# Kernel optimization log

Measured on AMD Instinct MI355X. Metric: run time of the kernel, lower is better.

## Reference

```python
import jax, jax.numpy as jnp
import numpy as np

N = 100000      # nodes
E = 3200000     # edges (avg degree 32)
DIN, DH, DOUT = 128, 32, 2


def setup_inputs() -> dict:
    key = jax.random.key(0)
    k1, k2, k3, k4 = jax.random.split(key, 4)
    x = jax.random.normal(k1, (N, DIN), dtype=jnp.float32)
    edge_index = jax.random.randint(k2, (2, E), 0, N, dtype=jnp.int64)
    # Glorot-ish scaled weights
    W1 = jax.random.normal(k3, (DIN, DH), dtype=jnp.float32) / np.sqrt(DIN)
    b1 = jnp.zeros((DH,), dtype=jnp.float32)
    W2 = jax.random.normal(k4, (DH, DOUT), dtype=jnp.float32) / np.sqrt(DH)
    b2 = jnp.zeros((DOUT,), dtype=jnp.float32)
    return {"x": x, "edge_index": edge_index, "W1": W1, "b1": b1, "W2": W2, "b2": b2}


def reference(x, edge_index, W1, b1, W2, b2):
    n = x.shape[0]
    # GCNConv default: add self-loops, symmetric deg^{-1/2} A deg^{-1/2} normalization
    loops = jnp.arange(n, dtype=edge_index.dtype)
    src = jnp.concatenate([edge_index[0], loops])  # [E+N]
    dst = jnp.concatenate([edge_index[1], loops])  # [E+N]
    deg = jax.ops.segment_sum(jnp.ones_like(dst, dtype=x.dtype), dst, num_segments=n)
    dinv = jnp.where(deg > 0, jax.lax.rsqrt(deg), 0.0)
    norm = dinv[src] * dinv[dst]  # [E+N]

    def gcn_layer(h, W, b):
        m = h @ W                                   # [n, dout] transform first (PyG order)
        msgs = m[src] * norm[:, None]               # gather + scale  [E+N, dout]
        agg = jax.ops.segment_sum(msgs, dst, num_segments=n)  # scatter-add
        return agg + b

    h = jax.nn.relu(gcn_layer(x, W1, b1))
    return gcn_layer(h, W2, b2)
```

## Files before the change

kernel.cpp:

```cpp
#include <hip/hip_runtime.h>
#include <hip/hip_bf16.h>

#define DIN 128
#define DH 32
#define DOUT 2
#define NPB 128
#define NPB_SHIFT 7
#define NBUK_MAX 1024
#define FILL_EDGES 8192
#define CHUNKB 8192


__device__ inline unsigned short f2bf(float f) {
    unsigned int u = __float_as_uint(f);
    u = (u + 0x7FFFu + ((u >> 16) & 1u)) >> 16;
    return (unsigned short)u;
}
__device__ inline float bf2f(unsigned short b) {
    return __uint_as_float(((unsigned int)b) << 16);
}
__device__ inline float bfLO(unsigned int w) { return __uint_as_float(w << 16); }
__device__ inline float bfHI(unsigned int w) { return __uint_as_float(w & 0xFFFF0000u); }

__global__ void zero_gcnt_kernel(int* __restrict__ gcnt, int nbuk) {
    int i = blockIdx.x * blockDim.x + threadIdx.x;
    if (i < nbuk) gcnt[i] = 0;
}

__global__ void bukhist_kernel(const int* __restrict__ dst, int* __restrict__ gcnt,
                               int e, int nbuk) {
    __shared__ int lcnt[NBUK_MAX];
    int t = threadIdx.x;
    for (int i = t; i < nbuk; i += 256) lcnt[i] = 0;
    __syncthreads();
    int e0 = blockIdx.x * FILL_EDGES;
    int m = min(FILL_EDGES, e - e0);
    for (int i = t; i < m; i += 256) atomicAdd(&lcnt[dst[e0 + i] >> NPB_SHIFT], 1);
    __syncthreads();
    for (int i = t; i < nbuk; i += 256)
        if (lcnt[i]) atomicAdd(&gcnt[i], lcnt[i]);
}

__global__ void scan_kernel(const int* __restrict__ gcnt, int* __restrict__ gbase,
                            int* __restrict__ gcur, int nbuk,
                            unsigned short* __restrict__ mqc, int n) {
    __shared__ int sd[256];
    int t = threadIdx.x;
    if (t < 16) ((unsigned int*)(mqc + (size_t)n * DH))[t] = 0u;
    int v[4], s = 0;
#pragma unroll
    for (int k = 0; k < 4; ++k) {
        int i = 4 * t + k;
        v[k] = (i < nbuk) ? gcnt[i] : 0;
        s += v[k];
    }
    sd[t] = s;
    __syncthreads();
    for (int off = 1; off < 256; off <<= 1) {
        int x = (t >= off) ? sd[t - off] : 0;
        __syncthreads();
        sd[t] += x;
        __syncthreads();
    }
    int run = sd[t] - s;
#pragma unroll
    for (int k = 0; k < 4; ++k) {
        int i = 4 * t + k;
        if (i < nbuk) { gbase[i] = run; gcur[i] = run; }
        run += v[k];
    }
}

__global__ void binfill_kernel(const int* __restrict__ src, const int* __restrict__ dst,
                               int* __restrict__ gcur, unsigned int* __restrict__ binned,
                               int e, int nbuk) {
    __shared__ int cnt[NBUK_MAX];
    __shared__ int pos[NBUK_MAX];
    __shared__ int gb[NBUK_MAX];
    __shared__ unsigned int sorted[FILL_EDGES];
    __shared__ unsigned short aux[FILL_EDGES];
    __shared__ int stmp[256];

    int t = threadIdx.x;
    int e0 = blockIdx.x * FILL_EDGES;
    int m = min(FILL_EDGES, e - e0);

    for (int i = t; i < nbuk; i += 256) cnt[i] = 0;
    __syncthreads();
    for (int i = t; i < m; i += 256) atomicAdd(&cnt[dst[e0 + i] >> NPB_SHIFT], 1);
    __syncthreads();

    int v[4], s = 0;
#pragma unroll
    for (int k = 0; k < 4; ++k) {
        int i = 4 * t + k;
        v[k] = (i < nbuk) ? cnt[i] : 0;
        s += v[k];
    }
    stmp[t] = s;
    __syncthreads();
    for (int off = 1; off < 256; off <<= 1) {
        int x = (t >= off) ? stmp[t - off] : 0;
        __syncthreads();
        stmp[t] += x;
        __syncthreads();
    }
    int run = stmp[t] - s;
#pragma unroll
    for (int k = 0; k < 4; ++k) {
        int i = 4 * t + k;
        if (i < nbuk) pos[i] = run;
        run += v[k];
    }
    __syncthreads();

    for (int i = t; i < m; i += 256) {
        int d = dst[e0 + i];
        int sv = src[e0 + i];
        int b = d >> NPB_SHIFT;
        int r = atomicAdd(&pos[b], 1);
        sorted[r] = ((unsigned int)(d & (NPB - 1)) << 17) | (unsigned int)sv;
        aux[r] = (unsigned short)b;
    }
    __syncthreads();

    for (int b = t; b < nbuk; b += 256) {
        int c = cnt[b];
        gb[b] = c ? atomicAdd(&gcur[b], c) : 0;
    }
    __syncthreads();

    for (int i = t; i < m; i += 256) {
        int b = aux[i];
        int start = pos[b] - cnt[b];
        binned[gb[b] + (i - start)] = sorted[i];
    }
}

__global__ void bdinv_kernel(const int* __restrict__ gbase, const int* __restrict__ gcnt,
                             const unsigned int* __restrict__ binned,
                             float* __restrict__ dinv, int* __restrict__ degarr, int n) {
    __shared__ int cnt[NPB];
    int t = threadIdx.x;
    int b = blockIdx.x;
    if (t < NPB) cnt[t] = 0;
    __syncthreads();
    const int beg = gbase[b];
    const int cntb = gcnt[b];
    for (int i = t; i < cntb; i += 256) atomicAdd(&cnt[binned[beg + i] >> 17], 1);
    __syncthreads();
    if (t < NPB) {
        int r = (b << NPB_SHIFT) + t;
        if (r < n) { dinv[r] = rsqrtf((float)(cnt[t] + 1)); degarr[r] = cnt[t]; }
    }
}

#define XLD 132
__global__ void gemm1_kernel(const float* __restrict__ x, const float* __restrict__ W1,
                             const float* __restrict__ dinv,
                             unsigned short* __restrict__ mqc, int n) {
    __shared__ float  Xl[32 * XLD];
    __shared__ float4 Wl4[DIN * 8];

    int t = threadIdx.x;
    for (int i = t; i < DIN * 8; i += 256) Wl4[i] = ((const float4*)W1)[i];

    int rb = blockIdx.x * 32;
    for (int i = t; i < 32 * 32; i += 256) {
        int rr = i >> 5, c4 = i & 31;
        int gr = rb + rr;
        float4 v = make_float4(0.f, 0.f, 0.f, 0.f);
        if (gr < n) v = ((const float4*)x)[(size_t)gr * 32 + c4];
        ((float4*)Xl)[rr * 33 + c4] = v;
    }
    __syncthreads();

    const int lane = t & 7;
    const int row  = t >> 3;
    const float* xrow = &Xl[row * XLD];
    float4 acc = make_float4(0.f, 0.f, 0.f, 0.f);
#pragma unroll
    for (int k = 0; k < DIN; ++k) {
        float xv = xrow[k];
        float4 w = Wl4[k * 8 + lane];
        acc.x += xv * w.x; acc.y += xv * w.y;
        acc.z += xv * w.z; acc.w += xv * w.w;
    }
    int r = rb + row;
    if (r < n) {
        float di = dinv[r];
        ushort4 sv;
        sv.x = f2bf(acc.x * di); sv.y = f2bf(acc.y * di);
        sv.z = f2bf(acc.z * di); sv.w = f2bf(acc.w * di);
        *(ushort4*)&mqc[(size_t)r * DH + 4 * lane] = sv;
    }
}

__global__ void __launch_bounds__(256, 3)
agg1_kernel(const int* __restrict__ gbase, const int* __restrict__ gcnt,
            const int* __restrict__ degarr,
            unsigned int* __restrict__ binned,
            const unsigned short* __restrict__ mqc,
            const float* __restrict__ dinv,
            const float* __restrict__ b1, const float* __restrict__ W2,
            float2* __restrict__ m2q, int n) {
    __shared__ unsigned int sortedc[CHUNKB];
    __shared__ int dg[NPB];
    __shared__ int coffs[NPB];
    __shared__ int poffs[NPB];
    __shared__ int cur[NPB];
    __shared__ int gmax[16];
    __shared__ int pbase[16];
    __shared__ int stmp[256];
    __shared__ int padtot;

    const int t = threadIdx.x;
    const int b = blockIdx.x;
    const int beg = gbase[b];
    const int cntb = gcnt[b];
    const int r0 = b << NPB_SHIFT;

    if (t < NPB) {
        int r = r0 + t;
        dg[t] = (r < n) ? degarr[r] : 0;
    }
    __syncthreads();

    if (t < 16) {
        int mx = 0;
#pragma unroll
        for (int k = 0; k < 8; ++k) mx = max(mx, dg[t * 8 + k]);
        gmax[t] = mx;
    }
    int v = (t < NPB) ? dg[t] : 0;
    stmp[t] = v;
    __syncthreads();

    if (t == 0) {
        int run = 0;
#pragma unroll
        for (int g = 0; g < 16; ++g) { pbase[g] = run; run += 8 * gmax[g]; }
        padtot = run;
    }
    for (int o = 1; o < NPB; o <<= 1) {
        int xx = (t >= o) ? stmp[t - o] : 0;
        __syncthreads();
        stmp[t] += xx;
        __syncthreads();
    }
    if (t < NPB) coffs[t] = stmp[t] - v;
    __syncthreads();

    if (padtot <= CHUNKB && cntb <= CHUNKB) {
        if (t < NPB) {
            int p = pbase[t >> 3] + (t & 7) * gmax[t >> 3];
            poffs[t] = p;
            cur[t] = p;
        }
        __syncthreads();

        for (int i = t; i < padtot; i += 256) sortedc[i] = (unsigned int)n;
        __syncthreads();
        for (int i = t; i < cntb; i += 256) {
            unsigned int en = binned[beg + i];
            int p = atomicAdd(&cur[en >> 17], 1);
            sortedc[p] = en & 0x1FFFFu;
        }
        __syncthreads();

        const int g = t >> 4, l = t & 15;
        const int mk = gmax[g];
        int bq[8];
#pragma unroll
        for (int q = 0; q < 8; ++q) bq[q] = poffs[g * 8 + q];

        float aLo[8], aHi[8];
#pragma unroll
        for (int q = 0; q < 8; ++q) { aLo[q] = 0.f; aHi[q] = 0.f; }

        for (int u = 0; u < mk; ++u) {
            unsigned int sv[8];
#pragma unroll
            for (int q = 0; q < 8; ++q) sv[q] = sortedc[bq[q] + u];
            unsigned int w[8];
#pragma unroll
            for (int q = 0; q < 8; ++q)
                w[q] = ((const unsigned int*)(mqc + (size_t)sv[q] * DH))[l];
#pragma unroll
            for (int q = 0; q < 8; ++q) {
                aLo[q] += bfLO(w[q]);
                aHi[q] += bfHI(w[q]);
            }
        }

        {
            int j = t >> 1, hf = t & 1;
            int d = dg[j], cb = coffs[j], pb = poffs[j];
            for (int k = hf; k < d; k += 2)
                binned[beg + cb + k] = sortedc[pb + k];
        }

        float2 bb = ((const float2*)b1)[l];
        float4 w4 = ((const float4*)W2)[l];
#pragma unroll
        for (int q = 0; q < 8; ++q) {
            int r = r0 + g * 8 + q;
            if (r < n) {
                float di = dinv[r];
                unsigned int sw = ((const unsigned int*)(mqc + (size_t)r * DH))[l];
                float h0 = fmaxf(di * (aLo[q] + bfLO(sw)) + bb.x, 0.0f);
                float h1 = fmaxf(di * (aHi[q] + bfHI(sw)) + bb.y, 0.0f);
                float p0 = h0 * w4.x + h1 * w4.z;
                float p1 = h0 * w4.y + h1 * w4.w;
#pragma unroll
                for (int o = 8; o > 0; o >>= 1) {
                    p0 += __shfl_down(p0, o, 16);
                    p1 += __shfl_down(p1, o, 16);
                }
                if (l == 0) m2q[r] = make_float2(di * p0, di * p1);
            }
        }
        return;
    }

    {
        const int lane = t & 31;
        const int half = t >> 5;
        float acc[16];
#pragma unroll
        for (int q = 0; q < 16; ++q) acc[q] = 0.0f;

        for (int off = 0; off < cntb; off += CHUNKB) {
            const int m = min(CHUNKB, cntb - off);

            if (t < NPB) cur[t] = 0;
            __syncthreads();
            for (int i = t; i < m; i += 256)
                atomicAdd(&cur[binned[beg + off + i] >> 17], 1);
            __syncthreads();

            int vv = (t < NPB) ? cur[t] : 0;
            stmp[t] = vv;
            __syncthreads();
            for (int o = 1; o < NPB; o <<= 1) {
                int xx = (t >= o) ? stmp[t - o] : 0;
                __syncthreads();
                stmp[t] += xx;
                __syncthreads();
            }
            if (t < NPB) { dg[t] = vv; poffs[t] = stmp[t] - vv; cur[t] = stmp[t] - vv; }
            __syncthreads();

            for (int i = t; i < m; i += 256) {
                unsigned int en = binned[beg + off + i];
                int p = atomicAdd(&cur[en >> 17], 1);
                sortedc[p] = en & 0x1FFFFu;
            }
            __syncthreads();

            int e0q[16], kq[16];
            int maxk = 0;
#pragma unroll
            for (int q = 0; q < 16; ++q) {
                int j = q * 8 + half;
                e0q[q] = poffs[j];
                kq[q] = dg[j];
                maxk = max(maxk, kq[q]);
            }
            for (int u = 0; u < maxk; ++u) {
                float val[16];
#pragma unroll
                for (int q = 0; q < 16; ++q) {
                    int idx = min(e0q[q] + u, m - 1);
                    int s = (int)sortedc[idx];
                    val[q] = bf2f(mqc[(size_t)s * DH + lane]);
                }
#pragma unroll
                for (int q = 0; q < 16; ++q)
                    acc[q] += (u < kq[q]) ? val[q] : 0.0f;
            }
            __syncthreads();
        }

#pragma unroll
        for (int q = 0; q < 16; ++q) {
            const int j = q * 8 + half;
            const int r = r0 + j;
            if (r < n) {
                float di = dinv[r];
                float a = acc[q] + bf2f(mqc[(size_t)r * DH + lane]);
                float h = fmaxf(di * a + b1[lane], 0.0f);
                float p0 = h * W2[lane * DOUT + 0];
                float p1 = h * W2[lane * DOUT + 1];
#pragma unroll
                for (int o = 16; o > 0; o >>= 1) {
                    p0 += __shfl_down(p0, o, 32);
                    p1 += __shfl_down(p1, o, 32);
                }
                if (lane == 0) m2q[r] = make_float2(di * p0, di * p1);
            }
        }
        if (cntb <= CHUNKB) {
            for (int i = t; i < cntb; i += 256) binned[beg + i] = sortedc[i];
        }
    }
}

__global__ void agg2_kernel(const int* __restrict__ gbase, const int* __restrict__ gcnt,
                            const int* __restrict__ degarr,
                            const unsigned int* __restrict__ binned,
                            const float2* __restrict__ m2q,
                            const float* __restrict__ dinv, const float* __restrict__ b2,
                            float* __restrict__ out, int n) {
    __shared__ int dg[NPB];
    __shared__ int offs[NPB];
    __shared__ int stmp[256];
    __shared__ float a0s[NPB], a1s[NPB];

    const int t = threadIdx.x;
    const int b = blockIdx.x;
    const int beg = gbase[b];
    const int cntb = gcnt[b];
    const int r0 = b << NPB_SHIFT;

    if (cntb <= CHUNKB) {
        if (t < NPB) {
            int r = r0 + t;
            dg[t] = (r < n) ? degarr[r] : 0;
        }
        __syncthreads();
        int v = (t < NPB) ? dg[t] : 0;
        stmp[t] = v;
        __syncthreads();
        for (int o = 1; o < NPB; o <<= 1) {
            int xx = (t >= o) ? stmp[t - o] : 0;
            __syncthreads();
            stmp[t] += xx;
            __syncthreads();
        }
        if (t < NPB) offs[t] = stmp[t] - v;
        __syncthreads();

        int j = t >> 1, hf = t & 1;
        int d = dg[j], o = offs[j];
        int lo = o + (hf ? (d >> 1) : 0);
        int hi = o + (hf ? d : (d >> 1));
        float a0 = 0.f, a1 = 0.f;
        for (int i = lo; i < hi; ++i) {
            int s = (int)(binned[beg + i] & 0x1FFFFu);
            float2 vv = m2q[s];
            a0 += vv.x; a1 += vv.y;
        }
        a0 += __shfl_down(a0, 1, 2);
        a1 += __shfl_down(a1, 1, 2);
        if (hf == 0) {
            int r = r0 + j;
            if (r < n) {
                float di = dinv[r];
                float2 self = m2q[r];
                out[(size_t)r * DOUT + 0] = di * (a0 + self.x) + b2[0];
                out[(size_t)r * DOUT + 1] = di * (a1 + self.y) + b2[1];
            }
        }
    } else {
        for (int i = t; i < NPB; i += 256) { a0s[i] = 0.f; a1s[i] = 0.f; }
        __syncthreads();
        for (int i = t; i < cntb; i += 256) {
            unsigned int entry = binned[beg + i];
            int sv = (int)(entry & 0x1FFFFu);
            int dl = (int)(entry >> 17);
            float2 vv = m2q[sv];
            atomicAdd(&a0s[dl], vv.x);
            atomicAdd(&a1s[dl], vv.y);
        }
        __syncthreads();
        for (int rl = t; rl < NPB; rl += 256) {
            int r = r0 + rl;
            if (r < n) {
                float di = dinv[r];
                float2 self = m2q[r];
                out[(size_t)r * DOUT + 0] = di * (a0s[rl] + self.x) + b2[0];
                out[(size_t)r * DOUT + 1] = di * (a1s[rl] + self.y) + b2[1];
            }
        }
    }
}

extern "C" void kernel_launch(void* const* d_in, const int* in_sizes, int n_in,
                              void* d_out, int out_size, void* d_ws, size_t ws_size,
                              hipStream_t stream) {
    const float* x  = (const float*)d_in[0];
    const int*   ei = (const int*)d_in[1];
    const float* W1 = (const float*)d_in[2];
    const float* b1 = (const float*)d_in[3];
    const float* W2 = (const float*)d_in[4];
    const float* b2 = (const float*)d_in[5];
    float* out = (float*)d_out;

    const int n = in_sizes[0] / DIN;
    const int e = in_sizes[1] / 2;
    const int* src = ei;
    const int* dst = ei + e;
    const int nbuk = (n + NPB - 1) >> NPB_SHIFT;

    char* ws = (char*)d_ws;
    float* dinv   = (float*)ws;          ws += (size_t)n * 4;
    int* degarr   = (int*)ws;            ws += (size_t)n * 4;
    int* gcnt     = (int*)ws;            ws += NBUK_MAX * 4;
    int* gbase    = (int*)ws;            ws += NBUK_MAX * 4;
    int* gcur     = (int*)ws;            ws += NBUK_MAX * 4;
    unsigned int* binned = (unsigned int*)ws;   ws += (size_t)e * 4;
    unsigned short* mqc  = (unsigned short*)ws; ws += ((size_t)n + 1) * DH * 2;
    float2* m2q   = (float2*)ws;

    const int B = 256;
    const int fill_blocks = (e + FILL_EDGES - 1) / FILL_EDGES;

    zero_gcnt_kernel<<<(nbuk + B - 1) / B, B, 0, stream>>>(gcnt, nbuk);
    bukhist_kernel<<<fill_blocks, B, 0, stream>>>(dst, gcnt, e, nbuk);
    scan_kernel<<<1, B, 0, stream>>>(gcnt, gbase, gcur, nbuk, mqc, n);
    binfill_kernel<<<fill_blocks, B, 0, stream>>>(src, dst, gcur, binned, e, nbuk);
    bdinv_kernel<<<nbuk, B, 0, stream>>>(gbase, gcnt, binned, dinv, degarr, n);
    gemm1_kernel<<<(n + 31) / 32, B, 0, stream>>>(x, W1, dinv, mqc, n);
    agg1_kernel<<<nbuk, B, 0, stream>>>(gbase, gcnt, degarr, binned, mqc, dinv, b1, W2, m2q, n);
    agg2_kernel<<<nbuk, B, 0, stream>>>(gbase, gcnt, degarr, binned, m2q, dinv, b2, out, n);
}
```

Before: 250.2 us.

## Replace per-bucket LDS sort with shared-memory atomic accumulation in aggregation

Both aggregation kernels drop the in-block counting sort of each bucket's edges (degree arrays, prefix scans, padded per-row slots, binned write-back). Instead they stream the bucket's binned edges directly, gather the source features, and accumulate them with LDS float atomics into a padded per-row accumulator. Edge loads become nontemporal and are unrolled by four, degarr is removed, and occupancy hints rise to 4. This cuts the sort and scan overhead and the write-back traffic, but adds LDS atomic contention and makes the summation order non-deterministic.

After: 882.9 us. 253% more time.

```diff
diff --git a/kernel.cpp b/kernel.cpp
--- a/kernel.cpp
+++ b/kernel.cpp
@@ -8,16 +8,12 @@
 #define NPB_SHIFT 7
 #define NBUK_MAX 1024
 #define FILL_EDGES 8192
-#define CHUNKB 8192
 
 
 __device__ inline unsigned short f2bf(float f) {
     unsigned int u = __float_as_uint(f);
     u = (u + 0x7FFFu + ((u >> 16) & 1u)) >> 16;
     return (unsigned short)u;
-}
-__device__ inline float bf2f(unsigned short b) {
-    return __uint_as_float(((unsigned int)b) << 16);
 }
 __device__ inline float bfLO(unsigned int w) { return __uint_as_float(w << 16); }
 __device__ inline float bfHI(unsigned int w) { return __uint_as_float(w & 0xFFFF0000u); }
@@ -139,7 +135,7 @@
 
 __global__ void bdinv_kernel(const int* __restrict__ gbase, const int* __restrict__ gcnt,
                              const unsigned int* __restrict__ binned,
-                             float* __restrict__ dinv, int* __restrict__ degarr, int n) {
+                             float* __restrict__ dinv, int n) {
     __shared__ int cnt[NPB];
     int t = threadIdx.x;
     int b = blockIdx.x;
@@ -151,7 +147,7 @@
     __syncthreads();
     if (t < NPB) {
         int r = (b << NPB_SHIFT) + t;
-        if (r < n) { dinv[r] = rsqrtf((float)(cnt[t] + 1)); degarr[r] = cnt[t]; }
+        if (r < n) dinv[r] = rsqrtf((float)(cnt[t] + 1));
     }
 }
 
@@ -196,23 +192,14 @@
     }
 }
 
-__global__ void __launch_bounds__(256, 3)
+__global__ void __launch_bounds__(256, 4)
 agg1_kernel(const int* __restrict__ gbase, const int* __restrict__ gcnt,
-            const int* __restrict__ degarr,
-            unsigned int* __restrict__ binned,
+            const unsigned int* __restrict__ binned,
             const unsigned short* __restrict__ mqc,
             const float* __restrict__ dinv,
             const float* __restrict__ b1, const float* __restrict__ W2,
             float2* __restrict__ m2q, int n) {
-    __shared__ unsigned int sortedc[CHUNKB];
-    __shared__ int dg[NPB];
-    __shared__ int coffs[NPB];
-    __shared__ int poffs[NPB];
-    __shared__ int cur[NPB];
-    __shared__ int gmax[16];
-    __shared__ int pbase[16];
-    __shared__ int stmp[256];
-    __shared__ int padtot;
+    __shared__ float acc[NPB * 33];
 
     const int t = threadIdx.x;
     const int b = blockIdx.x;
@@ -220,268 +207,108 @@
     const int cntb = gcnt[b];
     const int r0 = b << NPB_SHIFT;
 
-    if (t < NPB) {
-        int r = r0 + t;
-        dg[t] = (r < n) ? degarr[r] : 0;
-    }
-    __syncthreads();
-
-    if (t < 16) {
-        int mx = 0;
-#pragma unroll
-        for (int k = 0; k < 8; ++k) mx = max(mx, dg[t * 8 + k]);
-        gmax[t] = mx;
-    }
-    int v = (t < NPB) ? dg[t] : 0;
-    stmp[t] = v;
-    __syncthreads();
-
-    if (t == 0) {
-        int run = 0;
-#pragma unroll
-        for (int g = 0; g < 16; ++g) { pbase[g] = run; run += 8 * gmax[g]; }
-        padtot = run;
-    }
-    for (int o = 1; o < NPB; o <<= 1) {
-        int xx = (t >= o) ? stmp[t - o] : 0;
-        __syncthreads();
-        stmp[t] += xx;
-        __syncthreads();
-    }
-    if (t < NPB) coffs[t] = stmp[t] - v;
-    __syncthreads();
-
-    if (padtot <= CHUNKB && cntb <= CHUNKB) {
-        if (t < NPB) {
-            int p = pbase[t >> 3] + (t & 7) * gmax[t >> 3];
-            poffs[t] = p;
-            cur[t] = p;
+    for (int i = t; i < NPB * 33; i += 256) acc[i] = 0.f;
+    __syncthreads();
+
+    const int g = t >> 4, l = t & 15;
+    const unsigned int* __restrict__ bp = binned + beg;
+    const unsigned int* __restrict__ mq32 = (const unsigned int*)mqc;
+
+    int i = g;
+    for (; i + 48 < cntb; i += 64) {
+        unsigned int e0 = __builtin_nontemporal_load(&bp[i]);
+        unsigned int e1 = __builtin_nontemporal_load(&bp[i + 16]);
+        unsigned int e2 = __builtin_nontemporal_load(&bp[i + 32]);
+        unsigned int e3 = __builtin_nontemporal_load(&bp[i + 48]);
+        unsigned int w0 = mq32[(e0 & 0x1FFFFu) * 16u + l];
+        unsigned int w1 = mq32[(e1 & 0x1FFFFu) * 16u + l];
+        unsigned int w2 = mq32[(e2 & 0x1FFFFu) * 16u + l];
+        unsigned int w3 = mq32[(e3 & 0x1FFFFu) * 16u + l];
+        int d0 = (int)(e0 >> 17) * 33 + 2 * l;
+        int d1 = (int)(e1 >> 17) * 33 + 2 * l;
+        int d2 = (int)(e2 >> 17) * 33 + 2 * l;
+        int d3 = (int)(e3 >> 17) * 33 + 2 * l;
+        atomicAdd(&acc[d0], bfLO(w0)); atomicAdd(&acc[d0 + 1], bfHI(w0));
+        atomicAdd(&acc[d1], bfLO(w1)); atomicAdd(&acc[d1 + 1], bfHI(w1));
+        atomicAdd(&acc[d2], bfLO(w2)); atomicAdd(&acc[d2 + 1], bfHI(w2));
+        atomicAdd(&acc[d3], bfLO(w3)); atomicAdd(&acc[d3 + 1], bfHI(w3));
+    }
+    for (; i < cntb; i += 16) {
+        unsigned int e0 = __builtin_nontemporal_load(&bp[i]);
+        unsigned int w0 = mq32[(e0 & 0x1FFFFu) * 16u + l];
+        int d0 = (int)(e0 >> 17) * 33 + 2 * l;
+        atomicAdd(&acc[d0], bfLO(w0)); atomicAdd(&acc[d0 + 1], bfHI(w0));
+    }
+    __syncthreads();
+
+    const int j = t >> 1, hf = t & 1;
+    const int r = r0 + j;
+    if (r < n) {
+        const float di = dinv[r];
+        const unsigned int* srow = mq32 + (size_t)r * 16 + hf * 8;
+        const float* ar = &acc[j * 33 + hf * 16];
+        float p0 = 0.f, p1 = 0.f;
+#pragma unroll
+        for (int k = 0; k < 8; ++k) {
+            unsigned int sw = srow[k];
+            int c = hf * 16 + 2 * k;
+            float h0 = fmaxf(di * (ar[2 * k]     + bfLO(sw)) + b1[c],     0.0f);
+            float h1 = fmaxf(di * (ar[2 * k + 1] + bfHI(sw)) + b1[c + 1], 0.0f);
+            p0 += h0 * W2[2 * c]     + h1 * W2[2 * c + 2];
+            p1 += h0 * W2[2 * c + 1] + h1 * W2[2 * c + 3];
         }
-        __syncthreads();
-
-        for (int i = t; i < padtot; i += 256) sortedc[i] = (unsigned int)n;
-        __syncthreads();
-        for (int i = t; i < cntb; i += 256) {
-            unsigned int en = binned[beg + i];
-            int p = atomicAdd(&cur[en >> 17], 1);
-            sortedc[p] = en & 0x1FFFFu;
-        }
-        __syncthreads();
-
-        const int g = t >> 4, l = t & 15;
-        const int mk = gmax[g];
-        int bq[8];
-#pragma unroll
-        for (int q = 0; q < 8; ++q) bq[q] = poffs[g * 8 + q];
-
-        float aLo[8], aHi[8];
-#pragma unroll
-        for (int q = 0; q < 8; ++q) { aLo[q] = 0.f; aHi[q] = 0.f; }
-
-        for (int u = 0; u < mk; ++u) {
-            unsigned int sv[8];
-#pragma unroll
-            for (int q = 0; q < 8; ++q) sv[q] = sortedc[bq[q] + u];
-            unsigned int w[8];
-#pragma unroll
-            for (int q = 0; q < 8; ++q)
-                w[q] = ((const unsigned int*)(mqc + (size_t)sv[q] * DH))[l];
-#pragma unroll
-            for (int q = 0; q < 8; ++q) {
-                aLo[q] += bfLO(w[q]);
-                aHi[q] += bfHI(w[q]);
-            }
-        }
-
-        {
-            int j = t >> 1, hf = t & 1;
-            int d = dg[j], cb = coffs[j], pb = poffs[j];
-            for (int k = hf; k < d; k += 2)
-                binned[beg + cb + k] = sortedc[pb + k];
-        }
-
-        float2 bb = ((const float2*)b1)[l];
-        float4 w4 = ((const float4*)W2)[l];
-#pragma unroll
-        for (int q = 0; q < 8; ++q) {
-            int r = r0 + g * 8 + q;
-            if (r < n) {
-                float di = dinv[r];
-                unsigned int sw = ((const unsigned int*)(mqc + (size_t)r * DH))[l];
-                float h0 = fmaxf(di * (aLo[q] + bfLO(sw)) + bb.x, 0.0f);
-                float h1 = fmaxf(di * (aHi[q] + bfHI(sw)) + bb.y, 0.0f);
-                float p0 = h0 * w4.x + h1 * w4.z;
-                float p1 = h0 * w4.y + h1 * w4.w;
-#pragma unroll
-                for (int o = 8; o > 0; o >>= 1) {
-                    p0 += __shfl_down(p0, o, 16);
-                    p1 += __shfl_down(p1, o, 16);
-                }
-                if (l == 0) m2q[r] = make_float2(di * p0, di * p1);
-            }
-        }
-        return;
-    }
-
-    {
-        const int lane = t & 31;
-        const int half = t >> 5;
-        float acc[16];
-#pragma unroll
-        for (int q = 0; q < 16; ++q) acc[q] = 0.0f;
-
-        for (int off = 0; off < cntb; off += CHUNKB) {
-            const int m = min(CHUNKB, cntb - off);
-
-            if (t < NPB) cur[t] = 0;
-            __syncthreads();
-            for (int i = t; i < m; i += 256)
-                atomicAdd(&cur[binned[beg + off + i] >> 17], 1);
-            __syncthreads();
-
-            int vv = (t < NPB) ? cur[t] : 0;
-            stmp[t] = vv;
-            __syncthreads();
-            for (int o = 1; o < NPB; o <<= 1) {
-                int xx = (t >= o) ? stmp[t - o] : 0;
-                __syncthreads();
-                stmp[t] += xx;
-                __syncthreads();
-            }
-            if (t < NPB) { dg[t] = vv; poffs[t] = stmp[t] - vv; cur[t] = stmp[t] - vv; }
-            __syncthreads();
-
-            for (int i = t; i < m; i += 256) {
-                unsigned int en = binned[beg + off + i];
-                int p = atomicAdd(&cur[en >> 17], 1);
-                sortedc[p] = en & 0x1FFFFu;
-            }
-            __syncthreads();
-
-            int e0q[16], kq[16];
-            int maxk = 0;
-#pragma unroll
-            for (int q = 0; q < 16; ++q) {
-                int j = q * 8 + half;
-                e0q[q] = poffs[j];
-                kq[q] = dg[j];
-                maxk = max(maxk, kq[q]);
-            }
-            for (int u = 0; u < maxk; ++u) {
-                float val[16];
-#pragma unroll
-                for (int q = 0; q < 16; ++q) {
-                    int idx = min(e0q[q] + u, m - 1);
-                    int s = (int)sortedc[idx];
-                    val[q] = bf2f(mqc[(size_t)s * DH + lane]);
-                }
-#pragma unroll
-                for (int q = 0; q < 16; ++q)
-                    acc[q] += (u < kq[q]) ? val[q] : 0.0f;
-            }
-            __syncthreads();
-        }
-
-#pragma unroll
-        for (int q = 0; q < 16; ++q) {
-            const int j = q * 8 + half;
-            const int r = r0 + j;
-            if (r < n) {
-                float di = dinv[r];
-                float a = acc[q] + bf2f(mqc[(size_t)r * DH + lane]);
-                float h = fmaxf(di * a + b1[lane], 0.0f);
-                float p0 = h * W2[lane * DOUT + 0];
-                float p1 = h * W2[lane * DOUT + 1];
-#pragma unroll
-                for (int o = 16; o > 0; o >>= 1) {
-                    p0 += __shfl_down(p0, o, 32);
-                    p1 += __shfl_down(p1, o, 32);
-                }
-                if (lane == 0) m2q[r] = make_float2(di * p0, di * p1);
-            }
-        }
-        if (cntb <= CHUNKB) {
-            for (int i = t; i < cntb; i += 256) binned[beg + i] = sortedc[i];
-        }
-    }
-}
-
-__global__ void agg2_kernel(const int* __restrict__ gbase, const int* __restrict__ gcnt,
-                            const int* __restrict__ degarr,
-                            const unsigned int* __restrict__ binned,
-                            const float2* __restrict__ m2q,
-                            const float* __restrict__ dinv, const float* __restrict__ b2,
-                            float* __restrict__ out, int n) {
-    __shared__ int dg[NPB];
-    __shared__ int offs[NPB];
-    __shared__ int stmp[256];
+        p0 += __shfl_down(p0, 1, 2);
+        p1 += __shfl_down(p1, 1, 2);
+        if (hf == 0) m2q[r] = make_float2(di * p0, di * p1);
+    }
+}
+
+__global__ void __launch_bounds__(256, 4)
+agg2_kernel(const int* __restrict__ gbase, const int* __restrict__ gcnt,
+            const unsigned int* __restrict__ binned,
+            const float2* __restrict__ m2q,
+            const float* __restrict__ dinv, const float* __restrict__ b2,
+            float* __restrict__ out, int n) {
     __shared__ float a0s[NPB], a1s[NPB];
-
     const int t = threadIdx.x;
     const int b = blockIdx.x;
     const int beg = gbase[b];
     const int cntb = gcnt[b];
     const int r0 = b << NPB_SHIFT;
 
-    if (cntb <= CHUNKB) {
-        if (t < NPB) {
-            int r = r0 + t;
-            dg[t] = (r < n) ? degarr[r] : 0;
-        }
-        __syncthreads();
-        int v = (t < NPB) ? dg[t] : 0;
-        stmp[t] = v;
-        __syncthreads();
-        for (int o = 1; o < NPB; o <<= 1) {
-            int xx = (t >= o) ? stmp[t - o] : 0;
-            __syncthreads();
-            stmp[t] += xx;
-            __syncthreads();
-        }
-        if (t < NPB) offs[t] = stmp[t] - v;
-        __syncthreads();
-
-        int j = t >> 1, hf = t & 1;
-        int d = dg[j], o = offs[j];
-        int lo = o + (hf ? (d >> 1) : 0);
-        int hi = o + (hf ? d : (d >> 1));
-        float a0 = 0.f, a1 = 0.f;
-        for (int i = lo; i < hi; ++i) {
-            int s = (int)(binned[beg + i] & 0x1FFFFu);
-            float2 vv = m2q[s];
-            a0 += vv.x; a1 += vv.y;
-        }
-        a0 += __shfl_down(a0, 1, 2);
-        a1 += __shfl_down(a1, 1, 2);
-        if (hf == 0) {
-            int r = r0 + j;
-            if (r < n) {
-                float di = dinv[r];
-                float2 self = m2q[r];
-                out[(size_t)r * DOUT + 0] = di * (a0 + self.x) + b2[0];
-                out[(size_t)r * DOUT + 1] = di * (a1 + self.y) + b2[1];
-            }
-        }
-    } else {
-        for (int i = t; i < NPB; i += 256) { a0s[i] = 0.f; a1s[i] = 0.f; }
-        __syncthreads();
-        for (int i = t; i < cntb; i += 256) {
-            unsigned int entry = binned[beg + i];
-            int sv = (int)(entry & 0x1FFFFu);
-            int dl = (int)(entry >> 17);
-            float2 vv = m2q[sv];
-            atomicAdd(&a0s[dl], vv.x);
-            atomicAdd(&a1s[dl], vv.y);
-        }
-        __syncthreads();
-        for (int rl = t; rl < NPB; rl += 256) {
-            int r = r0 + rl;
-            if (r < n) {
-                float di = dinv[r];
-                float2 self = m2q[r];
-                out[(size_t)r * DOUT + 0] = di * (a0s[rl] + self.x) + b2[0];
-                out[(size_t)r * DOUT + 1] = di * (a1s[rl] + self.y) + b2[1];
-            }
+    if (t < NPB) { a0s[t] = 0.f; a1s[t] = 0.f; }
+    __syncthreads();
+
+    const unsigned int* __restrict__ bp = binned + beg;
+    int i = t;
+    for (; i + 768 < cntb; i += 1024) {
+        unsigned int e0 = __builtin_nontemporal_load(&bp[i]);
+        unsigned int e1 = __builtin_nontemporal_load(&bp[i + 256]);
+        unsigned int e2 = __builtin_nontemporal_load(&bp[i + 512]);
+        unsigned int e3 = __builtin_nontemporal_load(&bp[i + 768]);
+        float2 v0 = m2q[e0 & 0x1FFFFu];
+        float2 v1 = m2q[e1 & 0x1FFFFu];
+        float2 v2 = m2q[e2 & 0x1FFFFu];
+        float2 v3 = m2q[e3 & 0x1FFFFu];
+        atomicAdd(&a0s[e0 >> 17], v0.x); atomicAdd(&a1s[e0 >> 17], v0.y);
+        atomicAdd(&a0s[e1 >> 17], v1.x); atomicAdd(&a1s[e1 >> 17], v1.y);
+        atomicAdd(&a0s[e2 >> 17], v2.x); atomicAdd(&a1s[e2 >> 17], v2.y);
+        atomicAdd(&a0s[e3 >> 17], v3.x); atomicAdd(&a1s[e3 >> 17], v3.y);
+    }
+    for (; i < cntb; i += 256) {
+        unsigned int e0 = __builtin_nontemporal_load(&bp[i]);
+        float2 v0 = m2q[e0 & 0x1FFFFu];
+        atomicAdd(&a0s[e0 >> 17], v0.x); atomicAdd(&a1s[e0 >> 17], v0.y);
+    }
+    __syncthreads();
+
+    if (t < NPB) {
+        int r = r0 + t;
+        if (r < n) {
+            float di = dinv[r];
+            float2 self = m2q[r];
+            out[(size_t)r * DOUT + 0] = di * (a0s[t] + self.x) + b2[0];
+            out[(size_t)r * DOUT + 1] = di * (a1s[t] + self.y) + b2[1];
         }
     }
 }
@@ -505,7 +332,6 @@
 
     char* ws = (char*)d_ws;
     float* dinv   = (float*)ws;          ws += (size_t)n * 4;
-    int* degarr   = (int*)ws;            ws += (size_t)n * 4;
     int* gcnt     = (int*)ws;            ws += NBUK_MAX * 4;
     int* gbase    = (int*)ws;            ws += NBUK_MAX * 4;
     int* gcur     = (int*)ws;            ws += NBUK_MAX * 4;
@@ -520,8 +346,8 @@
     bukhist_kernel<<<fill_blocks, B, 0, stream>>>(dst, gcnt, e, nbuk);
     scan_kernel<<<1, B, 0, stream>>>(gcnt, gbase, gcur, nbuk, mqc, n);
     binfill_kernel<<<fill_blocks, B, 0, stream>>>(src, dst, gcur, binned, e, nbuk);
-    bdinv_kernel<<<nbuk, B, 0, stream>>>(gbase, gcnt, binned, dinv, degarr, n);
+    bdinv_kernel<<<nbuk, B, 0, stream>>>(gbase, gcnt, binned, dinv, n);
     gemm1_kernel<<<(n + 31) / 32, B, 0, stream>>>(x, W1, dinv, mqc, n);
-    agg1_kernel<<<nbuk, B, 0, stream>>>(gbase, gcnt, degarr, binned, mqc, dinv, b1, W2, m2q, n);
-    agg2_kernel<<<nbuk, B, 0, stream>>>(gbase, gcnt, degarr, binned, m2q, dinv, b2, out, n);
-}
+    agg1_kernel<<<nbuk, B, 0, stream>>>(gbase, gcnt, binned, mqc, dinv, b1, W2, m2q, n);
+    agg2_kernel<<<nbuk, B, 0, stream>>>(gbase, gcnt, binned, m2q, dinv, b2, out, n);
+}
```
